# Kernel optimization log

Measured on AMD Instinct MI355X. Metric: run time of the kernel, lower is better.

Reference implementation:

```python
import jax, jax.numpy as jnp
import numpy as np

N = 50000
E = 800000
IN = 256
H = 8
D = 32
NEG_SLOPE = 0.2


def setup_inputs() -> dict:
    key = jax.random.key(0)
    ks = jax.random.split(key, 16)
    inp = {
        "h": jax.random.normal(ks[0], (N, IN), jnp.float32),
        "src_a": jax.random.randint(ks[1], (E,), 0, N),
        "dst_a": jax.random.randint(ks[2], (E,), 0, N),
        "src_b": jax.random.randint(ks[3], (E,), 0, N),
        "dst_b": jax.random.randint(ks[4], (E,), 0, N),
        "W_a": jax.random.normal(ks[5], (IN, H * D), jnp.float32) * 0.05,
        "attn_l_a": jax.random.normal(ks[6], (H, D), jnp.float32) * 0.1,
        "attn_r_a": jax.random.normal(ks[7], (H, D), jnp.float32) * 0.1,
        "bias_a": jax.random.normal(ks[8], (H * D,), jnp.float32) * 0.1,
        "W_b": jax.random.normal(ks[9], (IN, H * D), jnp.float32) * 0.05,
        "attn_l_b": jax.random.normal(ks[10], (H, D), jnp.float32) * 0.1,
        "attn_r_b": jax.random.normal(ks[11], (H, D), jnp.float32) * 0.1,
        "bias_b": jax.random.normal(ks[12], (H * D,), jnp.float32) * 0.1,
        "sem_W1": jax.random.normal(ks[13], (H * D, 128), jnp.float32) * 0.05,
        "sem_b1": jnp.zeros((128,), jnp.float32),
        "sem_W2": jax.random.normal(ks[14], (128, 1), jnp.float32) * 0.1,
    }
    return inp


def gat_conv(h, src, dst, W, attn_l, attn_r, bias):
    # DGL GATConv: project, per-edge additive attention, segment softmax over dst, scatter-agg, bias, ELU
    feat = (h @ W).reshape(N, H, D)                      # [N,H,D]
    el = (feat * attn_l).sum(-1)                          # [N,H]
    er = (feat * attn_r).sum(-1)                          # [N,H]
    e = el[src] + er[dst]                                 # [E,H]
    e = jnp.where(e > 0, e, NEG_SLOPE * e)                # LeakyReLU(0.2)
    m = jax.ops.segment_max(e, dst, num_segments=N)       # [N,H] (-inf for empty)
    ex = jnp.exp(e - m[dst])                              # [E,H]
    denom = jax.ops.segment_sum(ex, dst, num_segments=N)  # [N,H]
    msg = feat[src] * ex[:, :, None]                      # [E,H,D]
    agg = jax.ops.segment_sum(msg, dst, num_segments=N)   # [N,H,D]
    safe = jnp.where(denom > 0, denom, 1.0)
    rst = agg / safe[:, :, None] + bias.reshape(1, H, D)
    rst = jnp.where(rst > 0, rst, jnp.expm1(rst))         # ELU
    return rst.reshape(N, H * D)


def semantic_attention(z, sem_W1, sem_b1, sem_W2):
    # z: [N, M, H*D]
    w = (jnp.tanh(z @ sem_W1 + sem_b1) @ sem_W2).mean(0)  # [M,1]
    beta = jax.nn.softmax(w, axis=0)                      # [M,1]
    return (beta[None] * z).sum(1)                        # [N, H*D]


def reference(h, src_a, dst_a, src_b, dst_b,
              W_a, attn_l_a, attn_r_a, bias_a,
              W_b, attn_l_b, attn_r_b, bias_b,
              sem_W1, sem_b1, sem_W2):
    z_a = gat_conv(h, src_a, dst_a, W_a, attn_l_a, attn_r_a, bias_a)
    z_b = gat_conv(h, src_b, dst_b, W_b, attn_l_b, attn_r_b, bias_b)
    z = jnp.stack([z_a, z_b], axis=1)                     # [N,2,H*D]
    return semantic_attention(z, sem_W1, sem_b1, sem_W2)
```

## Files before the change

### kernel.cpp

```cpp
#include <hip/hip_runtime.h>
#include <math.h>

typedef __attribute__((ext_vector_type(8))) short bf16x8;
typedef __attribute__((ext_vector_type(4))) float f32x4;
typedef __attribute__((ext_vector_type(4))) unsigned short us4;
typedef __attribute__((ext_vector_type(8))) unsigned short us8;

static constexpr int kN  = 50000;
static constexpr int kE  = 800000;
static constexpr int kNBUK = 98;
static constexpr int kCAP  = 9216;

__device__ __forceinline__ float b2f(unsigned short u) {
  union { unsigned u; float f; } x; x.u = ((unsigned)u) << 16; return x.f;
}
__device__ __forceinline__ unsigned short f2b(float f) {
  union { float f; unsigned u; } x; x.f = f;
  unsigned u = x.u;
  unsigned r = (u + 0x7fffu + ((u >> 16) & 1u)) >> 16;
  return (unsigned short)r;
}

__global__ __launch_bounds__(256)
void k_prep(const float* __restrict__ Wa, const float* __restrict__ Wb,
            const float* __restrict__ W1,
            unsigned short* __restrict__ wta, unsigned short* __restrict__ wtb,
            unsigned short* __restrict__ w1t) {
  int b = blockIdx.x, t = threadIdx.x;
  if (b < 256) {
    int i = b * 256 + t, j = i >> 8, k = i & 255;
    wta[j * 256 + k] = f2b(Wa[k * 256 + j]);
  } else if (b < 512) {
    int i = (b - 256) * 256 + t, j = i >> 8, k = i & 255;
    wtb[j * 256 + k] = f2b(Wb[k * 256 + j]);
  } else {
    int i = (b - 512) * 256 + t, j = i >> 8, k = i & 255;
    w1t[j * 256 + k] = f2b(W1[k * 128 + j]);
  }
}

__global__ __launch_bounds__(512, 2)
void k_gemm(const float* __restrict__ h,
            const unsigned short* __restrict__ wta,
            const unsigned short* __restrict__ wtb,
            const float* __restrict__ ala, const float* __restrict__ ara,
            const float* __restrict__ alb, const float* __restrict__ arb,
            unsigned short* __restrict__ fa, unsigned short* __restrict__ fb,
            float* __restrict__ ela, float* __restrict__ era,
            float* __restrict__ elb, float* __restrict__ erb) {
  __shared__ us8 la[64 * 8];
  __shared__ us8 lb[2][256 * 8];
  const int m0 = blockIdx.x * 64;
  const int t = threadIdx.x;
  const int lane = t & 63;
  const int wave = t >> 6;
  const int z = wave >> 2;
  const int col = lane & 15;
  const int quad = lane >> 4;
  const int nw = (wave & 3) * 64;
  unsigned short* f = z ? fb : fa;
  const float* al = z ? alb : ala;
  const float* ar = z ? arb : ara;
  float* el = z ? elb : ela;
  float* er = z ? erb : era;
  f32x4 acc[4][4];
#pragma unroll
  for (int i = 0; i < 4; ++i)
#pragma unroll
    for (int j = 0; j < 4; ++j) acc[i][j] = (f32x4){0.f, 0.f, 0.f, 0.f};

  for (int ks = 0; ks < 4; ++ks) {
    const int k0 = ks * 64;
    __syncthreads();
#pragma unroll
    for (int i = 0; i < 2; ++i) {
      int idx = i * 512 + t;
      int r = idx >> 4, g = (idx >> 1) & 7, half = idx & 1;
      int gr = m0 + r;
      f32x4 v = {0.f, 0.f, 0.f, 0.f};
      if (gr < kN) v = *(const f32x4*)(h + (size_t)gr * 256 + k0 + g * 8 + half * 4);
      us4 o;
      o.x = f2b(v.x); o.y = f2b(v.y); o.z = f2b(v.z); o.w = f2b(v.w);
      *(us4*)((unsigned short*)&la[r * 8 + (g ^ (r & 7))] + half * 4) = o;
    }
#pragma unroll
    for (int i = 0; i < 8; ++i) {
      int idx = i * 512 + t;
      int zz = idx >> 11;
      int id2 = idx & 2047;
      int r = id2 >> 3, g = id2 & 7;
      const unsigned short* w = zz ? wtb : wta;
      lb[zz][r * 8 + (g ^ (r & 7))] = *(const us8*)(w + r * 256 + k0 + g * 8);
    }
    __syncthreads();
#pragma unroll
    for (int k32 = 0; k32 < 64; k32 += 32) {
      const int cg = (k32 >> 3) + quad;
      bf16x8 af[4], bf[4];
#pragma unroll
      for (int s = 0; s < 4; ++s) {
        int arow = s * 16 + col;
        af[s] = (bf16x8)la[arow * 8 + (cg ^ (arow & 7))];
        int brow = nw + s * 16 + col;
        bf[s] = (bf16x8)lb[z][brow * 8 + (cg ^ (brow & 7))];
      }
#pragma unroll
      for (int i = 0; i < 4; ++i)
#pragma unroll
        for (int j = 0; j < 4; ++j)
          acc[i][j] = __builtin_amdgcn_mfma_f32_16x16x32_bf16(af[i], bf[j],
                                                              acc[i][j], 0, 0, 0);
    }
  }
#pragma unroll
  for (int i = 0; i < 4; ++i) {
#pragma unroll
    for (int r = 0; r < 4; ++r) {
      int row = m0 + i * 16 + quad * 4 + r;
      if (row < kN) {
#pragma unroll
        for (int j = 0; j < 4; ++j)
          f[(size_t)row * 256 + nw + j * 16 + col] = f2b(acc[i][j][r]);
      }
    }
  }
  float alv[4], arv[4];
#pragma unroll
  for (int j = 0; j < 4; ++j) {
    alv[j] = al[nw + j * 16 + col];
    arv[j] = ar[nw + j * 16 + col];
  }
  const int hA = nw >> 5;
#pragma unroll
  for (int i = 0; i < 4; ++i) {
#pragma unroll
    for (int r = 0; r < 4; ++r) {
      float pAl = acc[i][0][r] * alv[0] + acc[i][1][r] * alv[1];
      float pBl = acc[i][2][r] * alv[2] + acc[i][3][r] * alv[3];
      float pAr = acc[i][0][r] * arv[0] + acc[i][1][r] * arv[1];
      float pBr = acc[i][2][r] * arv[2] + acc[i][3][r] * arv[3];
#pragma unroll
      for (int off = 1; off < 16; off <<= 1) {
        pAl += __shfl_xor(pAl, off);
        pBl += __shfl_xor(pBl, off);
        pAr += __shfl_xor(pAr, off);
        pBr += __shfl_xor(pBr, off);
      }
      int row = m0 + i * 16 + quad * 4 + r;
      if (col == 0 && row < kN) {
        el[row * 8 + hA] = pAl;
        el[row * 8 + hA + 1] = pBl;
        er[row * 8 + hA] = pAr;
        er[row * 8 + hA + 1] = pBr;
      }
    }
  }
}

__global__ __launch_bounds__(256)
void k_part(const int* __restrict__ sa, const int* __restrict__ da,
            const int* __restrict__ sb, const int* __restrict__ db,
            int* __restrict__ cnt, unsigned* __restrict__ pay) {
  int y = blockIdx.y;
  const int* s = y ? sb : sa;
  const int* d = y ? db : da;
  unsigned* p = pay + (size_t)y * kNBUK * kCAP;
  int* cn = cnt + y * kNBUK;
  __shared__ unsigned stash[6400];
  __shared__ int h[kNBUK];
  int t = threadIdx.x;
  if (t < kNBUK) h[t] = 0;
  __syncthreads();
  int e0 = blockIdx.x * 6400;
#pragma unroll 5
  for (int it = 0; it < 25; ++it) {
    int e = e0 + it * 256 + t;
    int sv = s[e], dv = d[e];
    int b = dv >> 9;
    stash[it * 256 + t] = (unsigned)sv | ((unsigned)(dv & 511) << 16) |
                          ((unsigned)b << 25);
    atomicAdd(&h[b], 1);
  }
  __syncthreads();
  if (t < kNBUK) h[t] = atomicAdd(&cn[t], h[t]);
  __syncthreads();
#pragma unroll 5
  for (int it = 0; it < 25; ++it) {
    unsigned w = stash[it * 256 + t];
    int b = w >> 25;
    int slot = atomicAdd(&h[b], 1);
    p[b * kCAP + slot] = w & 0x1FFFFFFu;
  }
}

__global__ __launch_bounds__(256)
void k_bscan(const int* __restrict__ cnt, int* __restrict__ bbase,
             int* __restrict__ rpa, int* __restrict__ rpb) {
  __shared__ int buf[2][128];
  int t = threadIdx.x;
  int y = t >> 7, i = t & 127;
  int x = (i < kNBUK) ? cnt[y * kNBUK + i] : 0;
  buf[y][i] = x;
  __syncthreads();
  for (int off = 1; off < 128; off <<= 1) {
    int v = (i >= off) ? buf[y][i - off] : 0;
    __syncthreads();
    buf[y][i] += v;
    __syncthreads();
  }
  if (i < kNBUK) bbase[y * kNBUK + i] = buf[y][i] - x;
  if (t == 0) { rpa[kN] = kE; rpb[kN] = kE; }
}

__global__ __launch_bounds__(256)
void k_bucket(const int* __restrict__ cnt, const int* __restrict__ bbase,
              const unsigned* __restrict__ pay,
              int* __restrict__ rpa, int* __restrict__ rpb,
              int* __restrict__ esa, int* __restrict__ esb) {
  int b = blockIdx.x, y = blockIdx.y;
  int* rp = y ? rpb : rpa;
  int* es = y ? esb : esa;
  const unsigned* p = pay + ((size_t)y * kNBUK + b) * kCAP;
  int c = cnt[y * kNBUK + b];
  int base = bbase[y * kNBUK + b];
  __shared__ unsigned pl[kCAP];
  __shared__ int h[512];
  __shared__ int buf[256];
  int t = threadIdx.x;
  h[t] = 0; h[t + 256] = 0;
  __syncthreads();
  for (int i = t; i < c; i += 256) {
    unsigned w = p[i];
    pl[i] = w;
    atomicAdd(&h[(w >> 16) & 511], 1);
  }
  __syncthreads();
  int a = h[2 * t], b1 = h[2 * t + 1];
  int s2 = a + b1;
  buf[t] = s2;
  __syncthreads();
  for (int off = 1; off < 256; off <<= 1) {
    int v = (t >= off) ? buf[t - off] : 0;
    __syncthreads();
    buf[t] += v;
    __syncthreads();
  }
  int ex = buf[t] - s2;
  int g0 = b * 512 + 2 * t;
  if (g0 < kN) rp[g0] = base + ex;
  if (g0 + 1 < kN) rp[g0 + 1] = base + ex + a;
  h[2 * t] = ex;
  h[2 * t + 1] = ex + a;
  __syncthreads();
  for (int i = t; i < c; i += 256) {
    unsigned w = pl[i];
    int slot = atomicAdd(&h[(w >> 16) & 511], 1);
    es[base + slot] = (int)(w & 0xFFFFu);
  }
}

__global__ __launch_bounds__(256)
void k_agg(const int* __restrict__ rp, const int* __restrict__ es,
           const float* __restrict__ el, const float* __restrict__ er,
           const unsigned short* __restrict__ feat,
           const float* __restrict__ bias,
           float* __restrict__ za, unsigned short* __restrict__ zb,
           int y) {
  __shared__ float wls[4][512];
  __shared__ int sls[4][64];
  int nb = blockIdx.x;
  int lane = threadIdx.x & 63;
  int wave = threadIdx.x >> 6;
  int n = nb * 4 + wave;
  int hh = lane >> 3;
  int h = lane & 7;
  int half = lane >> 5;
  int l5 = lane & 31;
  int h2 = l5 >> 2;
  unsigned idx16 = (unsigned)l5 * 16u;
  float erh = er[n * 8 + h];
  int e0 = rp[n], e1 = rp[n + 1];
  float dsum = 0.f;
  float a0 = 0.f, a1 = 0.f, a2 = 0.f, a3 = 0.f;
  float a4 = 0.f, a5 = 0.f, a6 = 0.f, a7 = 0.f;

  for (int cb = e0; cb < e1; cb += 64) {
    int cnt = e1 - cb;
    if (cnt > 64) cnt = 64;
    for (int it = 0; it * 8 < cnt; ++it) {
      int j = it * 8 + hh;
      if (j < cnt) {
        int s = es[cb + j];
        float ev = *(const float*)((const char*)el + ((unsigned)s << 5) +
                                   ((unsigned)h << 2)) + erh;
        ev = fmaxf(ev, 0.2f * ev);
        float w = __expf(ev);
        wls[wave][it * 64 + lane] = w;
        if (h == 0) sls[wave][j] = s;
        dsum += w;
      }
    }
    int j = 0;
    for (; j + 7 < cnt; j += 8) {
#pragma unroll
      for (int p = 0; p < 4; ++p) {
        int jj = j + 2 * p + half;
        int s = sls[wave][jj];
        float w = wls[wave][jj * 8 + h2];
        us8 fv = *(const us8*)((const char*)feat + (((unsigned)s << 9) + idx16));
        a0 += w * b2f(fv[0]);
        a1 += w * b2f(fv[1]);
        a2 += w * b2f(fv[2]);
        a3 += w * b2f(fv[3]);
        a4 += w * b2f(fv[4]);
        a5 += w * b2f(fv[5]);
        a6 += w * b2f(fv[6]);
        a7 += w * b2f(fv[7]);
      }
    }
    if (j < cnt) {
#pragma unroll
      for (int p = 0; p < 4; ++p) {
        int jj = j + 2 * p + half;
        bool v = jj < cnt;
        int jc = v ? jj : j;
        int s = sls[wave][jc];
        float w = v ? wls[wave][jc * 8 + h2] : 0.f;
        us8 fv = *(const us8*)((const char*)feat + (((unsigned)s << 9) + idx16));
        a0 += w * b2f(fv[0]);
        a1 += w * b2f(fv[1]);
        a2 += w * b2f(fv[2]);
        a3 += w * b2f(fv[3]);
        a4 += w * b2f(fv[4]);
        a5 += w * b2f(fv[5]);
        a6 += w * b2f(fv[6]);
        a7 += w * b2f(fv[7]);
      }
    }
  }
  a0 += __shfl_xor(a0, 32); a1 += __shfl_xor(a1, 32);
  a2 += __shfl_xor(a2, 32); a3 += __shfl_xor(a3, 32);
  a4 += __shfl_xor(a4, 32); a5 += __shfl_xor(a5, 32);
  a6 += __shfl_xor(a6, 32); a7 += __shfl_xor(a7, 32);
  dsum += __shfl_xor(dsum, 8);
  dsum += __shfl_xor(dsum, 16);
  dsum += __shfl_xor(dsum, 32);
  float dh = __shfl(dsum, h2);
  float inv = __builtin_amdgcn_rcpf(dh > 0.f ? dh : 1.f);
  f32x4 blo = *(const f32x4*)(bias + l5 * 8);
  f32x4 bhi = *(const f32x4*)(bias + l5 * 8 + 4);
  float r0 = a0 * inv + blo.x;
  float r1 = a1 * inv + blo.y;
  float r2 = a2 * inv + blo.z;
  float r3 = a3 * inv + blo.w;
  float r4 = a4 * inv + bhi.x;
  float r5 = a5 * inv + bhi.y;
  float r6 = a6 * inv + bhi.z;
  float r7 = a7 * inv + bhi.w;
  r0 = r0 > 0.f ? r0 : __expf(r0) - 1.f;
  r1 = r1 > 0.f ? r1 : __expf(r1) - 1.f;
  r2 = r2 > 0.f ? r2 : __expf(r2) - 1.f;
  r3 = r3 > 0.f ? r3 : __expf(r3) - 1.f;
  r4 = r4 > 0.f ? r4 : __expf(r4) - 1.f;
  r5 = r5 > 0.f ? r5 : __expf(r5) - 1.f;
  r6 = r6 > 0.f ? r6 : __expf(r6) - 1.f;
  r7 = r7 > 0.f ? r7 : __expf(r7) - 1.f;
  f32x4 lo = {r0, r1, r2, r3};
  f32x4 hi = {r4, r5, r6, r7};
  f32x4 ov = half ? hi : lo;
  if (y == 0) {
    *(f32x4*)((char*)za + (size_t)n * 1024 + l5 * 32 + half * 16) = ov;
  } else {
    us4 o;
    o.x = f2b(ov.x); o.y = f2b(ov.y); o.z = f2b(ov.z); o.w = f2b(ov.w);
    *(us4*)((char*)zb + (size_t)n * 512 + l5 * 16 + half * 8) = o;
  }
}

__global__ __launch_bounds__(256)
void k_sem(const float* __restrict__ za,
           const unsigned short* __restrict__ zb,
           const unsigned short* __restrict__ w1t,
           const float* __restrict__ b1,
           const float* __restrict__ W2,
           float* __restrict__ wacc) {
  __shared__ us8 w1l[4096];
  int t = threadIdx.x;
  for (int i = t; i < 4096; i += 256) {
    int j = i >> 5, c = i & 31;
    w1l[j * 32 + (c ^ (j & 7))] = ((const us8*)w1t)[i];
  }
  __syncthreads();
  int lane = t & 63, wave = t >> 6;
  int col = lane & 15, quad = lane >> 4;
  float b1v[8], w2v[8];
#pragma unroll
  for (int tt = 0; tt < 8; ++tt) {
    b1v[tt] = b1[tt * 16 + col];
    w2v[tt] = W2[tt * 16 + col];
  }
  int gw = blockIdx.x * 4 + wave;
  int nw = gridDim.x * 4;
  float sa = 0.f, sb = 0.f;
  for (int gt = gw; gt < 6250; gt += nw) {
    f32x4 acc[8];
#pragma unroll
    for (int tt = 0; tt < 8; ++tt) acc[tt] = (f32x4){0.f, 0.f, 0.f, 0.f};
#pragma unroll
    for (int ks = 0; ks < 8; ++ks) {
      bf16x8 a;
      if (gt < 3125) {
        const float* ap = za + (size_t)gt * 4096 + col * 256 + ks * 32 + quad * 8;
        f32x4 a0 = *(const f32x4*)ap;
        f32x4 a1 = *(const f32x4*)(ap + 4);
        a[0] = (short)f2b(a0.x); a[1] = (short)f2b(a0.y);
        a[2] = (short)f2b(a0.z); a[3] = (short)f2b(a0.w);
        a[4] = (short)f2b(a1.x); a[5] = (short)f2b(a1.y);
        a[6] = (short)f2b(a1.z); a[7] = (short)f2b(a1.w);
      } else {
        a = *(const bf16x8*)(zb + (size_t)(gt - 3125) * 4096 + col * 256 +
                             ks * 32 + quad * 8);
      }
      int c = ks * 4 + quad;
#pragma unroll
      for (int tt = 0; tt < 8; ++tt) {
        int j = tt * 16 + col;
        bf16x8 b = (bf16x8)w1l[j * 32 + (c ^ (j & 7))];
        acc[tt] = __builtin_amdgcn_mfma_f32_16x16x32_bf16(a, b, acc[tt], 0, 0, 0);
      }
    }
    float tot = 0.f;
#pragma unroll
    for (int tt = 0; tt < 8; ++tt)
#pragma unroll
      for (int r = 0; r < 4; ++r) {
        float x = acc[tt][r] + b1v[tt];
        x = fminf(fmaxf(x, -10.f), 10.f);
        float ex = __expf(2.f * x);
        tot += (ex - 1.f) * __builtin_amdgcn_rcpf(ex + 1.f) * w2v[tt];
      }
#pragma unroll
    for (int off = 1; off < 64; off <<= 1) tot += __shfl_xor(tot, off);
    if (gt < 3125) sa += tot; else sb += tot;
  }
  if (lane == 0) {
    if (sa != 0.f) atomicAdd(&wacc[0], sa);
    if (sb != 0.f) atomicAdd(&wacc[1], sb);
  }
}

__global__ __launch_bounds__(256)
void k_combine(const float* __restrict__ za,
               const unsigned short* __restrict__ zb,
               const float* __restrict__ wacc,
               float* __restrict__ out) {
  int i = blockIdx.x * 256 + threadIdx.x;
  float wa = wacc[0] * (1.f / kN), wb = wacc[1] * (1.f / kN);
  float mx = fmaxf(wa, wb);
  float ea = __expf(wa - mx), eb = __expf(wb - mx);
  float inv = __builtin_amdgcn_rcpf(ea + eb);
  float ba = ea * inv, bb = eb * inv;
  f32x4 x = ((const f32x4*)za)[i];
  us4 yv = ((const us4*)zb)[i];
  f32x4 o;
#pragma unroll
  for (int j = 0; j < 4; ++j)
    o[j] = ba * x[j] + bb * b2f(yv[j]);
  ((f32x4*)out)[i] = o;
}

extern "C" void kernel_launch(void* const* d_in, const int* in_sizes, int n_in,
                              void* d_out, int out_size, void* d_ws, size_t ws_size,
                              hipStream_t stream) {
  const float* hin = (const float*)d_in[0];
  const int* src_a = (const int*)d_in[1];
  const int* dst_a = (const int*)d_in[2];
  const int* src_b = (const int*)d_in[3];
  const int* dst_b = (const int*)d_in[4];
  const float* W_a = (const float*)d_in[5];
  const float* al_a = (const float*)d_in[6];
  const float* ar_a = (const float*)d_in[7];
  const float* bias_a = (const float*)d_in[8];
  const float* W_b = (const float*)d_in[9];
  const float* al_b = (const float*)d_in[10];
  const float* ar_b = (const float*)d_in[11];
  const float* bias_b = (const float*)d_in[12];
  const float* sW1 = (const float*)d_in[13];
  const float* sb1 = (const float*)d_in[14];
  const float* sW2 = (const float*)d_in[15];
  float* out = (float*)d_out;

  char* wsb = (char*)d_ws;
  size_t off = 0;
  auto alloc = [&](size_t bytes) -> char* {
    char* p = wsb + off;
    off = (off + bytes + 511) & ~(size_t)511;
    return p;
  };
  unsigned short* feat_a = (unsigned short*)alloc((size_t)kN * 256 * 2);
  unsigned short* feat_b = (unsigned short*)alloc((size_t)kN * 256 * 2);
  unsigned short* z_b    = (unsigned short*)alloc((size_t)kN * 256 * 2);
  float* el_a = (float*)alloc((size_t)kN * 8 * 4);
  float* er_a = (float*)alloc((size_t)kN * 8 * 4);
  float* el_b = (float*)alloc((size_t)kN * 8 * 4);
  float* er_b = (float*)alloc((size_t)kN * 8 * 4);
  unsigned short* wt_a = (unsigned short*)alloc(65536 * 2);
  unsigned short* wt_b = (unsigned short*)alloc(65536 * 2);
  unsigned short* w1t  = (unsigned short*)alloc(32768 * 2);
  int* rp_a = (int*)alloc((size_t)(kN + 1) * 4);
  int* rp_b = (int*)alloc((size_t)(kN + 1) * 4);
  int* es_a = (int*)alloc((size_t)kE * 4);
  int* es_b = (int*)alloc((size_t)kE * 4);
  unsigned* pay = (unsigned*)alloc((size_t)2 * kNBUK * kCAP * 4);
  int* cnt = (int*)alloc((size_t)2 * kNBUK * 4);
  int* bbase = (int*)alloc((size_t)2 * kNBUK * 4);
  float* wacc = (float*)alloc(2 * 4);

  hipMemsetAsync(cnt, 0, (size_t)2 * kNBUK * 4, stream);
  hipMemsetAsync(wacc, 0, 8, stream);

  k_prep<<<640, 256, 0, stream>>>(W_a, W_b, sW1, wt_a, wt_b, w1t);
  k_part<<<dim3(125, 2), 256, 0, stream>>>(src_a, dst_a, src_b, dst_b, cnt, pay);
  k_bscan<<<1, 256, 0, stream>>>(cnt, bbase, rp_a, rp_b);
  k_bucket<<<dim3(kNBUK, 2), 256, 0, stream>>>(cnt, bbase, pay,
                                               rp_a, rp_b, es_a, es_b);
  k_gemm<<<782, 512, 0, stream>>>(hin, wt_a, wt_b,
                                  al_a, ar_a, al_b, ar_b,
                                  feat_a, feat_b,
                                  el_a, er_a, el_b, er_b);
  k_agg<<<12500, 256, 0, stream>>>(rp_a, es_a, el_a, er_a, feat_a, bias_a,
                                   out, z_b, 0);
  k_agg<<<12500, 256, 0, stream>>>(rp_b, es_b, el_b, er_b, feat_b, bias_b,
                                   out, z_b, 1);
  k_sem<<<512, 256, 0, stream>>>(out, z_b, w1t, sb1, sW2, wacc);
  k_combine<<<12500, 256, 0, stream>>>(out, z_b, wacc, out);
}
```

Measured before the change: 448.0 us.

## Split fused dual-projection GEMM into per-relation grid dimension with smaller tiles

The GEMM now launches a 2D grid, with blockIdx.y choosing the relation (a or b), instead of one block computing both projections. Each block holds one 256-column weight tile, and each of its 8 waves covers 32 columns (one head) with a 4x2 accumulator array, so the el/er reduction writes one head per wave. This cuts LDS and register use per block and raises the occupancy hint from 2 to 6 blocks, exposing more parallelism and latency hiding. The cost is that each h tile is now loaded from global memory and converted to bf16 twice, once per relation.

```diff
diff --git a/kernel.cpp b/kernel.cpp
--- a/kernel.cpp
+++ b/kernel.cpp
@@ -39,7 +39,7 @@
   }
 }
 
-__global__ __launch_bounds__(512, 2)
+__global__ __launch_bounds__(512, 6)
 void k_gemm(const float* __restrict__ h,
             const unsigned short* __restrict__ wta,
             const unsigned short* __restrict__ wtb,
@@ -49,25 +49,26 @@
             float* __restrict__ ela, float* __restrict__ era,
             float* __restrict__ elb, float* __restrict__ erb) {
   __shared__ us8 la[64 * 8];
-  __shared__ us8 lb[2][256 * 8];
-  const int m0 = blockIdx.x * 64;
-  const int t = threadIdx.x;
-  const int lane = t & 63;
-  const int wave = t >> 6;
-  const int z = wave >> 2;
-  const int col = lane & 15;
-  const int quad = lane >> 4;
-  const int nw = (wave & 3) * 64;
+  __shared__ us8 lbb[256 * 8];
+  const int z = blockIdx.y;
+  const unsigned short* wt = z ? wtb : wta;
   unsigned short* f = z ? fb : fa;
   const float* al = z ? alb : ala;
   const float* ar = z ? arb : ara;
   float* el = z ? elb : ela;
   float* er = z ? erb : era;
-  f32x4 acc[4][4];
+  const int m0 = blockIdx.x * 64;
+  const int t = threadIdx.x;
+  const int lane = t & 63;
+  const int wave = t >> 6;
+  const int col = lane & 15;
+  const int quad = lane >> 4;
+  const int nw = wave * 32;
+  f32x4 acc[4][2];
 #pragma unroll
   for (int i = 0; i < 4; ++i)
 #pragma unroll
-    for (int j = 0; j < 4; ++j) acc[i][j] = (f32x4){0.f, 0.f, 0.f, 0.f};
+    for (int j = 0; j < 2; ++j) acc[i][j] = (f32x4){0.f, 0.f, 0.f, 0.f};
 
   for (int ks = 0; ks < 4; ++ks) {
     const int k0 = ks * 64;
@@ -84,30 +85,30 @@
       *(us4*)((unsigned short*)&la[r * 8 + (g ^ (r & 7))] + half * 4) = o;
     }
 #pragma unroll
-    for (int i = 0; i < 8; ++i) {
+    for (int i = 0; i < 4; ++i) {
       int idx = i * 512 + t;
-      int zz = idx >> 11;
-      int id2 = idx & 2047;
-      int r = id2 >> 3, g = id2 & 7;
-      const unsigned short* w = zz ? wtb : wta;
-      lb[zz][r * 8 + (g ^ (r & 7))] = *(const us8*)(w + r * 256 + k0 + g * 8);
+      int r = idx >> 3, g = idx & 7;
+      lbb[r * 8 + (g ^ (r & 7))] = *(const us8*)(wt + r * 256 + k0 + g * 8);
     }
     __syncthreads();
 #pragma unroll
     for (int k32 = 0; k32 < 64; k32 += 32) {
       const int cg = (k32 >> 3) + quad;
-      bf16x8 af[4], bf[4];
+      bf16x8 af[4], bf[2];
 #pragma unroll
       for (int s = 0; s < 4; ++s) {
         int arow = s * 16 + col;
         af[s] = (bf16x8)la[arow * 8 + (cg ^ (arow & 7))];
-        int brow = nw + s * 16 + col;
-        bf[s] = (bf16x8)lb[z][brow * 8 + (cg ^ (brow & 7))];
+      }
+#pragma unroll
+      for (int j = 0; j < 2; ++j) {
+        int brow = nw + j * 16 + col;
+        bf[j] = (bf16x8)lbb[brow * 8 + (cg ^ (brow & 7))];
       }
 #pragma unroll
       for (int i = 0; i < 4; ++i)
 #pragma unroll
-        for (int j = 0; j < 4; ++j)
+        for (int j = 0; j < 2; ++j)
           acc[i][j] = __builtin_amdgcn_mfma_f32_16x16x32_bf16(af[i], bf[j],
                                                               acc[i][j], 0, 0, 0);
     }
@@ -119,39 +120,32 @@
       int row = m0 + i * 16 + quad * 4 + r;
       if (row < kN) {
 #pragma unroll
-        for (int j = 0; j < 4; ++j)
+        for (int j = 0; j < 2; ++j)
           f[(size_t)row * 256 + nw + j * 16 + col] = f2b(acc[i][j][r]);
       }
     }
   }
-  float alv[4], arv[4];
-#pragma unroll
-  for (int j = 0; j < 4; ++j) {
+  float alv[2], arv[2];
+#pragma unroll
+  for (int j = 0; j < 2; ++j) {
     alv[j] = al[nw + j * 16 + col];
     arv[j] = ar[nw + j * 16 + col];
   }
-  const int hA = nw >> 5;
 #pragma unroll
   for (int i = 0; i < 4; ++i) {
 #pragma unroll
     for (int r = 0; r < 4; ++r) {
-      float pAl = acc[i][0][r] * alv[0] + acc[i][1][r] * alv[1];
-      float pBl = acc[i][2][r] * alv[2] + acc[i][3][r] * alv[3];
-      float pAr = acc[i][0][r] * arv[0] + acc[i][1][r] * arv[1];
-      float pBr = acc[i][2][r] * arv[2] + acc[i][3][r] * arv[3];
+      float pl = acc[i][0][r] * alv[0] + acc[i][1][r] * alv[1];
+      float pr = acc[i][0][r] * arv[0] + acc[i][1][r] * arv[1];
 #pragma unroll
       for (int off = 1; off < 16; off <<= 1) {
-        pAl += __shfl_xor(pAl, off);
-        pBl += __shfl_xor(pBl, off);
-        pAr += __shfl_xor(pAr, off);
-        pBr += __shfl_xor(pBr, off);
+        pl += __shfl_xor(pl, off);
+        pr += __shfl_xor(pr, off);
       }
       int row = m0 + i * 16 + quad * 4 + r;
       if (col == 0 && row < kN) {
-        el[row * 8 + hA] = pAl;
-        el[row * 8 + hA + 1] = pBl;
-        er[row * 8 + hA] = pAr;
-        er[row * 8 + hA + 1] = pBr;
+        el[row * 8 + wave] = pl;
+        er[row * 8 + wave] = pr;
       }
     }
   }
@@ -524,10 +518,10 @@
   k_bscan<<<1, 256, 0, stream>>>(cnt, bbase, rp_a, rp_b);
   k_bucket<<<dim3(kNBUK, 2), 256, 0, stream>>>(cnt, bbase, pay,
                                                rp_a, rp_b, es_a, es_b);
-  k_gemm<<<782, 512, 0, stream>>>(hin, wt_a, wt_b,
-                                  al_a, ar_a, al_b, ar_b,
-                                  feat_a, feat_b,
-                                  el_a, er_a, el_b, er_b);
+  k_gemm<<<dim3(782, 2), 512, 0, stream>>>(hin, wt_a, wt_b,
+                                           al_a, ar_a, al_b, ar_b,
+                                           feat_a, feat_b,
+                                           el_a, er_a, el_b, er_b);
   k_agg<<<12500, 256, 0, stream>>>(rp_a, es_a, el_a, er_a, feat_a, bias_a,
                                    out, z_b, 0);
   k_agg<<<12500, 256, 0, stream>>>(rp_b, es_b, el_b, er_b, feat_b, bias_b,
```

After: 444.7 us. Within noise of the previous version (-0.7%).
